# Kernel optimization log

Measured on AMD Instinct MI355X. Metric: run time of the kernel, lower is better.

The kernel has to match this reference:

```python
import jax, jax.numpy as jnp
import numpy as np

N_NODES = 100_000
N_EDGES = 3_200_000
N_FEAT = 128
N_HID = 8
N_CLASSES = 10


def setup_inputs() -> dict:
    key = jax.random.key(0)
    ks = jax.random.split(key, 16)
    g = lambda k, shape, fan_in: jax.random.normal(k, shape, jnp.float32) / np.sqrt(fan_in)
    inp = {}
    inp['x'] = jax.random.normal(ks[0], (N_NODES, N_FEAT), jnp.float32)
    inp['edge_index'] = jax.random.randint(ks[1], (2, N_EDGES), 0, N_NODES, jnp.int32)
    # lin: Linear(F, 8)
    inp['lin_w'] = g(ks[2], (N_FEAT, N_HID), N_FEAT)
    inp['lin_b'] = jnp.zeros((N_HID,), jnp.float32)
    # conv1: GATConv(8, 8, heads=2)
    inp['w1'] = g(ks[3], (N_HID, 2 * N_HID), N_HID)
    inp['a1_src'] = g(ks[4], (2, N_HID), N_HID)
    inp['a1_dst'] = g(ks[5], (2, N_HID), N_HID)
    inp['b1'] = jnp.zeros((2 * N_HID,), jnp.float32)
    # conv2: GATConv(16, 8, heads=2)
    inp['w2'] = g(ks[6], (2 * N_HID, 2 * N_HID), 2 * N_HID)
    inp['a2_src'] = g(ks[7], (2, N_HID), N_HID)
    inp['a2_dst'] = g(ks[8], (2, N_HID), N_HID)
    inp['b2'] = jnp.zeros((2 * N_HID,), jnp.float32)
    # conv3: GATConv(16, num_classes, heads=1, concat=False)
    inp['w3'] = g(ks[9], (2 * N_HID, N_CLASSES), 2 * N_HID)
    inp['a3_src'] = g(ks[10], (1, N_CLASSES), N_CLASSES)
    inp['a3_dst'] = g(ks[11], (1, N_CLASSES), N_CLASSES)
    inp['b3'] = jnp.zeros((N_CLASSES,), jnp.float32)
    return inp


def _gat_conv(x, W, a_src, a_dst, b, src, dst, heads, out_c, concat):
    """PyG GATConv with pre-appended self-loops in (src, dst)."""
    N = x.shape[0]
    xl = (x @ W).reshape(N, heads, out_c)                 # [N,H,C]
    alpha_src = (xl * a_src[None]).sum(-1)                # [N,H]
    alpha_dst = (xl * a_dst[None]).sum(-1)                # [N,H]
    e = jax.nn.leaky_relu(alpha_src[src] + alpha_dst[dst], 0.2)  # [E,H]
    # segment softmax over destination nodes
    m = jax.ops.segment_max(e, dst, num_segments=N)
    e = jnp.exp(e - m[dst])
    s = jax.ops.segment_sum(e, dst, num_segments=N)
    alpha = e / s[dst]                                    # [E,H]
    msg = xl[src] * alpha[:, :, None]                     # [E,H,C]
    out = jax.ops.segment_sum(msg, dst, num_segments=N)   # [N,H,C]
    out = out.reshape(N, heads * out_c) if concat else out.mean(axis=1)
    return out + b


def reference(x, edge_index, lin_w, lin_b, w1, a1_src, a1_dst, b1,
              w2, a2_src, a2_dst, b2, w3, a3_src, a3_dst, b3):
    N = x.shape[0]
    loops = jnp.arange(N, dtype=edge_index.dtype)
    src = jnp.concatenate([edge_index[0], loops])
    dst = jnp.concatenate([edge_index[1], loops])
    lrelu = lambda v: jax.nn.leaky_relu(v, 0.01)
    h = lrelu(x @ lin_w + lin_b)
    h = lrelu(_gat_conv(h, w1, a1_src, a1_dst, b1, src, dst, 2, N_HID, True))
    h = lrelu(_gat_conv(h, w2, a2_src, a2_dst, b2, src, dst, 2, N_HID, True))
    h = _gat_conv(h, w3, a3_src, a3_dst, b3, src, dst, 1, N_CLASSES, False)
    return jax.nn.log_softmax(h, axis=-1)
```

## Files before the change

### kernel.cpp

```cpp
#include <hip/hip_runtime.h>
#include <hip/hip_fp16.h>
#include <math.h>

#define N_NODES 100000
#define N_EDGES 3200000
#define ET (N_EDGES + N_NODES)
#define SLOT 80
#define KMAX 5
#define SHIFT 8
#define BNODES 256
#define NBUCK 391
#define BCAP 9088
#define P1_T 1024
#define E_PER 16
#define P1_WG ((N_EDGES + P1_T * E_PER - 1) / (P1_T * E_PER))
#define SCAN_T 1024
#define SCAN_CHUNK 98
#define LOG2E 1.44269504088896f

typedef _Float16 h2 __attribute__((ext_vector_type(2)));

__device__ __forceinline__ float lrelu(float v, float s) { return v > 0.f ? v : v * s; }
__device__ __forceinline__ float fexp2(float x) { return __builtin_amdgcn_exp2f(x); }

__device__ __forceinline__ h2 f2h2(float f) {
    union { float f; h2 h; } u; u.f = f; return u.h;
}

__device__ __forceinline__ float fdot2(h2 a, h2 b, float c) {
#if __has_builtin(__builtin_amdgcn_fdot2)
    return __builtin_amdgcn_fdot2(a, b, c, false);
#else
    return c + (float)a.x * (float)b.x + (float)a.y * (float)b.y;
#endif
}

template <int CTRL>
__device__ __forceinline__ float dppmov(float v) {
    return __int_as_float(__builtin_amdgcn_update_dpp(0, __float_as_int(v), CTRL, 0xF, 0xF, true));
}

__device__ __forceinline__ void reduce8(float a[8], float& ssum, int lane) {
    int b0 = lane & 1, b1 = (lane >> 1) & 1, b2 = (lane >> 2) & 1;
    float q0 = (b0 ? a[4] : a[0]) + dppmov<0xB1>(b0 ? a[0] : a[4]);
    float q1 = (b0 ? a[5] : a[1]) + dppmov<0xB1>(b0 ? a[1] : a[5]);
    float q2 = (b0 ? a[6] : a[2]) + dppmov<0xB1>(b0 ? a[2] : a[6]);
    float q3 = (b0 ? a[7] : a[3]) + dppmov<0xB1>(b0 ? a[3] : a[7]);
    float r0 = (b1 ? q2 : q0) + dppmov<0x4E>(b1 ? q0 : q2);
    float r1 = (b1 ? q3 : q1) + dppmov<0x4E>(b1 ? q1 : q3);
    float t  = (b2 ? r1 : r0) + __shfl_xor(b2 ? r0 : r1, 4, 64);
    t += __shfl_xor(t, 8, 64);
    a[0] = t;
    ssum += dppmov<0xB1>(ssum);
    ssum += dppmov<0x4E>(ssum);
    ssum += __shfl_xor(ssum, 4, 64);
    ssum += __shfl_xor(ssum, 8, 64);
}

__global__ void __launch_bounds__(P1_T) part_kernel(const int* __restrict__ ei,
                                                    int* __restrict__ bcur,
                                                    unsigned* __restrict__ pairs) {
    __shared__ int hist[NBUCK];
    __shared__ int gbase[NBUCK];
    int t = threadIdx.x;
    for (int i = t; i < NBUCK; i += P1_T) hist[i] = 0;
    __syncthreads();
    int base = blockIdx.x * (P1_T * E_PER);
    int s[E_PER], d[E_PER], r[E_PER];
#pragma unroll
    for (int k = 0; k < E_PER; k++) {
        int e = base + k * P1_T + t;
        if (e < N_EDGES) {
            s[k] = ei[e];
            d[k] = ei[N_EDGES + e];
            r[k] = atomicAdd(&hist[d[k] >> SHIFT], 1);
        }
    }
    __syncthreads();
    for (int i = t; i < NBUCK; i += P1_T)
        gbase[i] = (hist[i] > 0) ? atomicAdd(&bcur[i], hist[i]) : 0;
    __syncthreads();
#pragma unroll
    for (int k = 0; k < E_PER; k++) {
        int e = base + k * P1_T + t;
        if (e < N_EDGES) {
            int b = d[k] >> SHIFT;
            int pos = gbase[b] + r[k];
            if (pos < BCAP)
                pairs[(size_t)b * BCAP + pos] =
                    ((unsigned)(d[k] & (BNODES - 1)) << 17) | (unsigned)s[k];
        }
    }
}

__global__ void build_kernel(const int* __restrict__ bcur, const unsigned* __restrict__ pairs,
                             int* __restrict__ csr, int* __restrict__ deg) {
    __shared__ int offs[BNODES];
    int b = blockIdx.x;
    int t = threadIdx.x;
    int node0 = b << SHIFT;
    int n = node0 + t;
    if (n < N_NODES) {
        csr[n * SLOT] = n;
        offs[t] = 1;
    } else offs[t] = 0;
    __syncthreads();
    int cnt = min(bcur[b], BCAP);
    for (int i = t; i < cnt; i += BNODES) {
        unsigned v = pairs[(size_t)b * BCAP + i];
        int ln = v >> 17;
        int s = v & 0x1FFFF;
        int pos = atomicAdd(&offs[ln], 1);
        if (pos < SLOT) csr[(node0 + ln) * SLOT + pos] = s;
    }
    __syncthreads();
    if (n < N_NODES) deg[n] = offs[t];
}

__global__ void count_kernel(const int* __restrict__ ei, int* __restrict__ deg) {
    int e = blockIdx.x * blockDim.x + threadIdx.x;
    if (e >= ET) return;
    int d = (e < N_EDGES) ? ei[N_EDGES + e] : (e - N_EDGES);
    atomicAdd(&deg[d], 1);
}

__global__ void scan_kernel(const int* __restrict__ deg, int* __restrict__ rowptr,
                            int* __restrict__ cursor) {
    __shared__ int sums[SCAN_T];
    int t = threadIdx.x;
    int start = t * SCAN_CHUNK;
    int end = min(start + SCAN_CHUNK, N_NODES);
    int s = 0;
    for (int i = start; i < end; i++) s += deg[i];
    sums[t] = s;
    __syncthreads();
    for (int off = 1; off < SCAN_T; off <<= 1) {
        int v = sums[t];
        int add = (t >= off) ? sums[t - off] : 0;
        __syncthreads();
        sums[t] = v + add;
        __syncthreads();
    }
    int base = (t > 0) ? sums[t - 1] : 0;
    for (int i = start; i < end; i++) {
        rowptr[i] = base;
        cursor[i] = base;
        base += deg[i];
    }
    if (t == SCAN_T - 1) rowptr[N_NODES] = base;
}

__global__ void scatter_kernel(const int* __restrict__ ei, int* __restrict__ cursor,
                               int* __restrict__ csr) {
    int e = blockIdx.x * blockDim.x + threadIdx.x;
    if (e >= ET) return;
    int s, d;
    if (e < N_EDGES) { s = ei[e]; d = ei[N_EDGES + e]; } else { s = d = e - N_EDGES; }
    int pos = atomicAdd(&cursor[d], 1);
    csr[pos] = s;
}

template <int CIN, int H, int C, int XLS>
__global__ void prep_kernel(const float* __restrict__ hin, const float* __restrict__ W,
                            const float* __restrict__ a_src, const float* __restrict__ a_dst,
                            __half* __restrict__ xl, float* __restrict__ asrc,
                            float* __restrict__ adst) {
    __shared__ float Ws[CIN * H * C];
    __shared__ float As[H * C];
    __shared__ float Ad[H * C];
    for (int i = threadIdx.x; i < CIN * H * C; i += blockDim.x) Ws[i] = W[i];
    for (int i = threadIdx.x; i < H * C; i += blockDim.x) {
        As[i] = a_src[i] * LOG2E;
        Ad[i] = a_dst[i] * LOG2E;
    }
    __syncthreads();
    int n = blockIdx.x * blockDim.x + threadIdx.x;
    if (n >= N_NODES) return;
    float hreg[CIN];
#pragma unroll
    for (int i = 0; i < CIN; i += 4) {
        float4 v = *(const float4*)&hin[n * CIN + i];
        hreg[i] = v.x; hreg[i + 1] = v.y; hreg[i + 2] = v.z; hreg[i + 3] = v.w;
    }
#pragma unroll
    for (int h = 0; h < H; h++) {
        float as = 0.f, ad = 0.f;
#pragma unroll
        for (int c = 0; c < C; c++) {
            float v = 0.f;
#pragma unroll
            for (int i = 0; i < CIN; i++) v += hreg[i] * Ws[i * H * C + h * C + c];
            xl[n * XLS + h * C + c] = __float2half_rn(v);
            as += v * As[h * C + c];
            ad += v * Ad[h * C + c];
        }
        asrc[n * H + h] = as;
        adst[n * H + h] = ad;
    }
#pragma unroll
    for (int c = H * C; c < XLS; c++) xl[n * XLS + c] = __float2half_rn(0.f);
}

template <int H, int C, int XLS>
__global__ __launch_bounds__(256) void prep_lin_kernel(
        const float* __restrict__ x, const float* __restrict__ lw, const float* __restrict__ lb,
        const float* __restrict__ W, const float* __restrict__ a_src,
        const float* __restrict__ a_dst, __half* __restrict__ xl,
        float* __restrict__ asrc, float* __restrict__ adst) {
    __shared__ float LW[128 * 8];
    __shared__ float Ws[8 * H * C];
    __shared__ float As[H * C];
    __shared__ float Ad[H * C];
    __shared__ float Lb[8];
    for (int i = threadIdx.x; i < 128 * 8; i += 256) LW[i] = lw[i];
    for (int i = threadIdx.x; i < 8 * H * C; i += 256) Ws[i] = W[i];
    for (int i = threadIdx.x; i < H * C; i += 256) {
        As[i] = a_src[i] * LOG2E;
        Ad[i] = a_dst[i] * LOG2E;
    }
    if (threadIdx.x < 8) Lb[threadIdx.x] = lb[threadIdx.x];
    __syncthreads();
    int n = blockIdx.x * blockDim.x + threadIdx.x;
    if (n >= N_NODES) return;
    float hreg[8];
#pragma unroll
    for (int c = 0; c < 8; c++) hreg[c] = 0.f;
#pragma unroll 8
    for (int i = 0; i < 128; i += 4) {
        float4 v = *(const float4*)&x[n * 128 + i];
#pragma unroll
        for (int c = 0; c < 8; c++) hreg[c] += v.x * LW[(i + 0) * 8 + c];
#pragma unroll
        for (int c = 0; c < 8; c++) hreg[c] += v.y * LW[(i + 1) * 8 + c];
#pragma unroll
        for (int c = 0; c < 8; c++) hreg[c] += v.z * LW[(i + 2) * 8 + c];
#pragma unroll
        for (int c = 0; c < 8; c++) hreg[c] += v.w * LW[(i + 3) * 8 + c];
    }
#pragma unroll
    for (int c = 0; c < 8; c++) hreg[c] = lrelu(hreg[c] + Lb[c], 0.01f);
#pragma unroll
    for (int h = 0; h < H; h++) {
        float as = 0.f, ad = 0.f;
#pragma unroll
        for (int c = 0; c < C; c++) {
            float v = 0.f;
#pragma unroll
            for (int i = 0; i < 8; i++) v += hreg[i] * Ws[i * H * C + h * C + c];
            xl[n * XLS + h * C + c] = __float2half_rn(v);
            as += v * As[h * C + c];
            ad += v * Ad[h * C + c];
        }
        asrc[n * H + h] = as;
        adst[n * H + h] = ad;
    }
#pragma unroll
    for (int c = H * C; c < XLS; c++) xl[n * XLS + c] = __float2half_rn(0.f);
}

__global__ __launch_bounds__(256) void gat64_h2(const int* __restrict__ cnt_,
                                                const int* __restrict__ csr,
                                                const float* __restrict__ a_src,
                                                const float* __restrict__ adst,
                                                const __half* __restrict__ xl,
                                                const float* __restrict__ b,
                                                float* __restrict__ hout) {
    int wg = blockIdx.x * 4 + (threadIdx.x >> 6);
    int lane = threadIdx.x & 63;
    int eg = lane & 15;
    int q  = (lane >> 4) & 1;
    int nd = lane >> 5;
    int n = wg * 2 + nd;
    float4 as0 = *(const float4*)&a_src[q * 8];
    float4 as1 = *(const float4*)&a_src[q * 8 + 4];
    h2 av0 = {(_Float16)(as0.x * LOG2E), (_Float16)(as0.y * LOG2E)};
    h2 av1 = {(_Float16)(as0.z * LOG2E), (_Float16)(as0.w * LOG2E)};
    h2 av2 = {(_Float16)(as1.x * LOG2E), (_Float16)(as1.y * LOG2E)};
    h2 av3 = {(_Float16)(as1.z * LOG2E), (_Float16)(as1.w * LOG2E)};
    int cnt = min(cnt_[n], SLOT);
    float ad = adst[n * 2 + q];
    int idx[KMAX];
#pragma unroll
    for (int k = 0; k < KMAX; k++) {
        int i = eg + (k << 4);
        idx[k] = (i < cnt) ? csr[n * SLOT + i] : -1;
    }
    float ssum = 0.f;
    float a[8] = {0.f, 0.f, 0.f, 0.f, 0.f, 0.f, 0.f, 0.f};
#pragma unroll
    for (int k = 0; k < KMAX; k++) {
        int s = idx[k];
        if (s >= 0) {
            float4 raw = *(const float4*)&xl[s * 16 + q * 8];
            h2 x0 = f2h2(raw.x), x1 = f2h2(raw.y), x2 = f2h2(raw.z), x3 = f2h2(raw.w);
            float e = fdot2(x0, av0, fdot2(x1, av1, fdot2(x2, av2, fdot2(x3, av3, ad))));
            float w = fexp2(fmaxf(e, 0.2f * e));
            ssum += w;
            a[0] += w * (float)x0.x; a[1] += w * (float)x0.y;
            a[2] += w * (float)x1.x; a[3] += w * (float)x1.y;
            a[4] += w * (float)x2.x; a[5] += w * (float)x2.y;
            a[6] += w * (float)x3.x; a[7] += w * (float)x3.y;
        }
    }
    reduce8(a, ssum, lane);
    if ((lane & 8) == 0) {
        int ch = 8 * q + 4 * (lane & 1) + 2 * ((lane >> 1) & 1) + ((lane >> 2) & 1);
        hout[n * 16 + ch] = lrelu(a[0] / ssum + b[ch], 0.01f);
    }
}

__global__ __launch_bounds__(256) void gat64_ls(const int* __restrict__ cnt_,
                                                const int* __restrict__ csr,
                                                const float* __restrict__ a_src,
                                                const float* __restrict__ adst,
                                                const __half* __restrict__ xl,
                                                const float* __restrict__ b,
                                                float* __restrict__ out) {
    int wg = blockIdx.x * 4 + (threadIdx.x >> 6);
    int lane = threadIdx.x & 63;
    int eg = lane & 15;
    int q  = (lane >> 4) & 1;
    int nd = lane >> 5;
    int n = wg * 2 + nd;
    float avf[8];
#pragma unroll
    for (int j = 0; j < 8; j++) {
        int c = q * 8 + j;
        avf[j] = (c < 10) ? a_src[c] * LOG2E : 0.f;
    }
    h2 av0 = {(_Float16)avf[0], (_Float16)avf[1]};
    h2 av1 = {(_Float16)avf[2], (_Float16)avf[3]};
    h2 av2 = {(_Float16)avf[4], (_Float16)avf[5]};
    h2 av3 = {(_Float16)avf[6], (_Float16)avf[7]};
    int cnt = min(cnt_[n], SLOT);
    float adh = adst[n] * 0.5f;
    int idx[KMAX];
#pragma unroll
    for (int k = 0; k < KMAX; k++) {
        int i = eg + (k << 4);
        idx[k] = (i < cnt) ? csr[n * SLOT + i] : -1;
    }
    float ssum = 0.f;
    float a[8] = {0.f, 0.f, 0.f, 0.f, 0.f, 0.f, 0.f, 0.f};
#pragma unroll
    for (int k = 0; k < KMAX; k++) {
        int s = idx[k];
        if (s >= 0) {
            float4 raw = *(const float4*)&xl[s * 16 + q * 8];
            h2 x0 = f2h2(raw.x), x1 = f2h2(raw.y), x2 = f2h2(raw.z), x3 = f2h2(raw.w);
            float part = fdot2(x0, av0, fdot2(x1, av1, fdot2(x2, av2, fdot2(x3, av3, adh))));
            float e = part + __shfl_xor(part, 16, 64);
            float w = fexp2(fmaxf(e, 0.2f * e));
            ssum += w;
            a[0] += w * (float)x0.x; a[1] += w * (float)x0.y;
            a[2] += w * (float)x1.x; a[3] += w * (float)x1.y;
            a[4] += w * (float)x2.x; a[5] += w * (float)x2.y;
            a[6] += w * (float)x3.x; a[7] += w * (float)x3.y;
        }
    }
    reduce8(a, ssum, lane);
    int ch = 8 * q + 4 * (lane & 1) + 2 * ((lane >> 1) & 1) + ((lane >> 2) & 1);
    float u = (ch < 10) ? a[0] / ssum + b[ch] : -INFINITY;
    float m = u;
    m = fmaxf(m, dppmov<0xB1>(m));
    m = fmaxf(m, dppmov<0x4E>(m));
    m = fmaxf(m, __shfl_xor(m, 4, 64));
    m = fmaxf(m, __shfl_xor(m, 8, 64));
    m = fmaxf(m, __shfl_xor(m, 16, 64));
    float ex = (ch < 10 && (lane & 8) == 0) ? __expf(u - m) : 0.f;
    ex += dppmov<0xB1>(ex);
    ex += dppmov<0x4E>(ex);
    ex += __shfl_xor(ex, 4, 64);
    ex += __shfl_xor(ex, 8, 64);
    ex += __shfl_xor(ex, 16, 64);
    float lse = m + __logf(ex);
    if ((lane & 8) == 0 && ch < 10) out[n * 10 + ch] = u - lse;
}

__global__ void gat16_h2(const int* __restrict__ rowptr, const int* __restrict__ csr,
                         const float* __restrict__ asrc, const float* __restrict__ adst,
                         const __half* __restrict__ xl, const float* __restrict__ b,
                         float* __restrict__ hout) {
    int tid = blockIdx.x * blockDim.x + threadIdx.x;
    int wave = tid >> 6;
    int lane = threadIdx.x & 63;
    int g = lane >> 4;
    int c = lane & 15;
    int h = c >> 3;
    int n = wave * 4 + g;
    if (n >= N_NODES) return;
    int beg = rowptr[n], cnt = rowptr[n + 1] - beg;
    float adn = adst[n * 2 + h];
    float ssum = 0.f, pa = 0.f;
#pragma unroll 4
    for (int i = 0; i < cnt; i++) {
        int s = csr[beg + i];
        float e = asrc[s * 2 + h] + adn;
        float w = fexp2(fmaxf(e, 0.2f * e));
        ssum += w;
        pa += w * __half2float(xl[s * 16 + c]);
    }
    hout[n * 16 + c] = lrelu(pa / ssum + b[c], 0.01f);
}

__global__ void gat16_ls(const int* __restrict__ rowptr, const int* __restrict__ csr,
                         const float* __restrict__ asrc, const float* __restrict__ adst,
                         const __half* __restrict__ xl, const float* __restrict__ b,
                         float* __restrict__ out) {
    int tid = blockIdx.x * blockDim.x + threadIdx.x;
    int wave = tid >> 6;
    int lane = threadIdx.x & 63;
    int g = lane >> 4;
    int c = lane & 15;
    int n = wave * 4 + g;
    if (n >= N_NODES) return;
    int beg = rowptr[n], cnt = rowptr[n + 1] - beg;
    float adn = adst[n];
    float ssum = 0.f, pa = 0.f;
#pragma unroll 4
    for (int i = 0; i < cnt; i++) {
        int s = csr[beg + i];
        float e = asrc[s] + adn;
        float w = fexp2(fmaxf(e, 0.2f * e));
        ssum += w;
        pa += w * __half2float(xl[s * 16 + c]);
    }
    float v = pa / ssum + ((c < 10) ? b[c] : 0.f);
    float vm = (c < 10) ? v : -INFINITY;
#pragma unroll
    for (int off = 8; off >= 1; off >>= 1) vm = fmaxf(vm, __shfl_xor(vm, off, 16));
    float ex = (c < 10) ? __expf(v - vm) : 0.f;
    float sum = ex;
#pragma unroll
    for (int off = 8; off >= 1; off >>= 1) sum += __shfl_xor(sum, off, 16);
    float lse = vm + __logf(sum);
    if (c < 10) out[n * 10 + c] = v - lse;
}

extern "C" void kernel_launch(void* const* d_in, const int* in_sizes, int n_in,
                              void* d_out, int out_size, void* d_ws, size_t ws_size,
                              hipStream_t stream) {
    const float* x     = (const float*)d_in[0];
    const int*   ei    = (const int*)d_in[1];
    const float* lin_w = (const float*)d_in[2];
    const float* lin_b = (const float*)d_in[3];
    const float* w1    = (const float*)d_in[4];
    const float* a1s   = (const float*)d_in[5];
    const float* a1d   = (const float*)d_in[6];
    const float* b1    = (const float*)d_in[7];
    const float* w2    = (const float*)d_in[8];
    const float* a2s   = (const float*)d_in[9];
    const float* a2d   = (const float*)d_in[10];
    const float* b2    = (const float*)d_in[11];
    const float* w3    = (const float*)d_in[12];
    const float* a3s   = (const float*)d_in[13];
    const float* a3d   = (const float*)d_in[14];
    const float* b3    = (const float*)d_in[15];

    float* ws = (float*)d_ws;
    float* slotH  = ws;
    __half* slotX = (__half*)(ws + 1600000);
    float* as_    = ws + 3200000;
    float* ad_    = ws + 3400000;
    unsigned* pairs = (unsigned*)ws;
    int* csrP = (int*)(ws + 3600000);
    int* degP = (int*)(ws + 3600000 + N_NODES * SLOT);
    int* bcur = degP + N_NODES;
    size_t need_new = (size_t)(3600000 + N_NODES * SLOT + N_NODES + 512) * 4;

    int use_bucket = (ws_size >= need_new) ? 1 : 0;

    int* degC    = (int*)(ws + 3600000);
    int* rowptrC = degC + N_NODES;
    int* cursorC = rowptrC + N_NODES + 1;
    int* csrC    = cursorC + N_NODES;

    dim3 B(256);
    int nb_n  = (N_NODES + 255) / 256;
    int nb_et = (ET + 255) / 256;
    int nb_g  = (N_NODES + 15) / 16;
    int nb_w2 = N_NODES / 8;

    if (use_bucket) {
        hipMemsetAsync(bcur, 0, 512 * sizeof(int), stream);
        part_kernel<<<P1_WG, P1_T, 0, stream>>>(ei, bcur, pairs);
        build_kernel<<<NBUCK, BNODES, 0, stream>>>(bcur, pairs, csrP, degP);
    } else {
        hipMemsetAsync(degC, 0, N_NODES * sizeof(int), stream);
        count_kernel<<<nb_et, B, 0, stream>>>(ei, degC);
        scan_kernel<<<1, SCAN_T, 0, stream>>>(degC, rowptrC, cursorC);
        scatter_kernel<<<nb_et, B, 0, stream>>>(ei, cursorC, csrC);
    }

    prep_lin_kernel<2, 8, 16><<<nb_n, B, 0, stream>>>(x, lin_w, lin_b, w1, a1s, a1d,
                                                      slotX, as_, ad_);
    if (use_bucket) gat64_h2<<<nb_w2, B, 0, stream>>>(degP, csrP, a1s, ad_, slotX, b1, slotH);
    else            gat16_h2<<<nb_g, B, 0, stream>>>(rowptrC, csrC, as_, ad_, slotX, b1, slotH);

    prep_kernel<16, 2, 8, 16><<<nb_n, B, 0, stream>>>(slotH, w2, a2s, a2d, slotX, as_, ad_);
    if (use_bucket) gat64_h2<<<nb_w2, B, 0, stream>>>(degP, csrP, a2s, ad_, slotX, b2, slotH);
    else            gat16_h2<<<nb_g, B, 0, stream>>>(rowptrC, csrC, as_, ad_, slotX, b2, slotH);

    prep_kernel<16, 1, 10, 16><<<nb_n, B, 0, stream>>>(slotH, w3, a3s, a3d, slotX, as_, ad_);
    if (use_bucket) gat64_ls<<<nb_w2, B, 0, stream>>>(degP, csrP, a3s, ad_, slotX, b3, (float*)d_out);
    else            gat16_ls<<<nb_g, B, 0, stream>>>(rowptrC, csrC, as_, ad_, slotX, b3, (float*)d_out);
}
```

Baseline: 280.9 us.

## Replace two-pass bucketed CSR build with direct atomic slot scatter

The two-pass graph build (a bucket partition kernel with shared-memory histograms, then a per-bucket build kernel) is replaced by one kernel in which each edge atomically bumps its destination's degree and writes its source into a fixed-width slot row. The self-loop is no longer stored in the slot array; the GAT kernels add it implicitly as index zero and shift the stored neighbours by one. This removes a kernel launch and the intermediate pairs buffer, but relies on scattered global atomics across 100k counters and uncoalesced writes into the slot array.

```diff
diff --git a/kernel.cpp b/kernel.cpp
--- a/kernel.cpp
+++ b/kernel.cpp
@@ -7,13 +7,6 @@
 #define ET (N_EDGES + N_NODES)
 #define SLOT 80
 #define KMAX 5
-#define SHIFT 8
-#define BNODES 256
-#define NBUCK 391
-#define BCAP 9088
-#define P1_T 1024
-#define E_PER 16
-#define P1_WG ((N_EDGES + P1_T * E_PER - 1) / (P1_T * E_PER))
 #define SCAN_T 1024
 #define SCAN_CHUNK 98
 #define LOG2E 1.44269504088896f
@@ -57,64 +50,14 @@
     ssum += __shfl_xor(ssum, 8, 64);
 }
 
-__global__ void __launch_bounds__(P1_T) part_kernel(const int* __restrict__ ei,
-                                                    int* __restrict__ bcur,
-                                                    unsigned* __restrict__ pairs) {
-    __shared__ int hist[NBUCK];
-    __shared__ int gbase[NBUCK];
-    int t = threadIdx.x;
-    for (int i = t; i < NBUCK; i += P1_T) hist[i] = 0;
-    __syncthreads();
-    int base = blockIdx.x * (P1_T * E_PER);
-    int s[E_PER], d[E_PER], r[E_PER];
-#pragma unroll
-    for (int k = 0; k < E_PER; k++) {
-        int e = base + k * P1_T + t;
-        if (e < N_EDGES) {
-            s[k] = ei[e];
-            d[k] = ei[N_EDGES + e];
-            r[k] = atomicAdd(&hist[d[k] >> SHIFT], 1);
-        }
-    }
-    __syncthreads();
-    for (int i = t; i < NBUCK; i += P1_T)
-        gbase[i] = (hist[i] > 0) ? atomicAdd(&bcur[i], hist[i]) : 0;
-    __syncthreads();
-#pragma unroll
-    for (int k = 0; k < E_PER; k++) {
-        int e = base + k * P1_T + t;
-        if (e < N_EDGES) {
-            int b = d[k] >> SHIFT;
-            int pos = gbase[b] + r[k];
-            if (pos < BCAP)
-                pairs[(size_t)b * BCAP + pos] =
-                    ((unsigned)(d[k] & (BNODES - 1)) << 17) | (unsigned)s[k];
-        }
-    }
-}
-
-__global__ void build_kernel(const int* __restrict__ bcur, const unsigned* __restrict__ pairs,
-                             int* __restrict__ csr, int* __restrict__ deg) {
-    __shared__ int offs[BNODES];
-    int b = blockIdx.x;
-    int t = threadIdx.x;
-    int node0 = b << SHIFT;
-    int n = node0 + t;
-    if (n < N_NODES) {
-        csr[n * SLOT] = n;
-        offs[t] = 1;
-    } else offs[t] = 0;
-    __syncthreads();
-    int cnt = min(bcur[b], BCAP);
-    for (int i = t; i < cnt; i += BNODES) {
-        unsigned v = pairs[(size_t)b * BCAP + i];
-        int ln = v >> 17;
-        int s = v & 0x1FFFF;
-        int pos = atomicAdd(&offs[ln], 1);
-        if (pos < SLOT) csr[(node0 + ln) * SLOT + pos] = s;
-    }
-    __syncthreads();
-    if (n < N_NODES) deg[n] = offs[t];
+__global__ void scatter_slot(const int* __restrict__ ei, int* __restrict__ deg,
+                             int* __restrict__ csr) {
+    int e = blockIdx.x * blockDim.x + threadIdx.x;
+    if (e >= N_EDGES) return;
+    int s = ei[e];
+    int d = ei[N_EDGES + e];
+    int pos = atomicAdd(&deg[d], 1);
+    if (pos < SLOT - 1) csr[d * SLOT + pos] = s;
 }
 
 __global__ void count_kernel(const int* __restrict__ ei, int* __restrict__ deg) {
@@ -277,13 +220,14 @@
     h2 av1 = {(_Float16)(as0.z * LOG2E), (_Float16)(as0.w * LOG2E)};
     h2 av2 = {(_Float16)(as1.x * LOG2E), (_Float16)(as1.y * LOG2E)};
     h2 av3 = {(_Float16)(as1.z * LOG2E), (_Float16)(as1.w * LOG2E)};
-    int cnt = min(cnt_[n], SLOT);
+    int cnt = min(cnt_[n] + 1, SLOT);
     float ad = adst[n * 2 + q];
     int idx[KMAX];
 #pragma unroll
     for (int k = 0; k < KMAX; k++) {
         int i = eg + (k << 4);
-        idx[k] = (i < cnt) ? csr[n * SLOT + i] : -1;
+        int j = i ? i - 1 : 0;
+        idx[k] = (i < cnt) ? (i ? csr[n * SLOT + j] : n) : -1;
     }
     float ssum = 0.f;
     float a[8] = {0.f, 0.f, 0.f, 0.f, 0.f, 0.f, 0.f, 0.f};
@@ -332,13 +276,14 @@
     h2 av1 = {(_Float16)avf[2], (_Float16)avf[3]};
     h2 av2 = {(_Float16)avf[4], (_Float16)avf[5]};
     h2 av3 = {(_Float16)avf[6], (_Float16)avf[7]};
-    int cnt = min(cnt_[n], SLOT);
+    int cnt = min(cnt_[n] + 1, SLOT);
     float adh = adst[n] * 0.5f;
     int idx[KMAX];
 #pragma unroll
     for (int k = 0; k < KMAX; k++) {
         int i = eg + (k << 4);
-        idx[k] = (i < cnt) ? csr[n * SLOT + i] : -1;
+        int j = i ? i - 1 : 0;
+        idx[k] = (i < cnt) ? (i ? csr[n * SLOT + j] : n) : -1;
     }
     float ssum = 0.f;
     float a[8] = {0.f, 0.f, 0.f, 0.f, 0.f, 0.f, 0.f, 0.f};
@@ -462,10 +407,8 @@
     __half* slotX = (__half*)(ws + 1600000);
     float* as_    = ws + 3200000;
     float* ad_    = ws + 3400000;
-    unsigned* pairs = (unsigned*)ws;
     int* csrP = (int*)(ws + 3600000);
     int* degP = (int*)(ws + 3600000 + N_NODES * SLOT);
-    int* bcur = degP + N_NODES;
     size_t need_new = (size_t)(3600000 + N_NODES * SLOT + N_NODES + 512) * 4;
 
     int use_bucket = (ws_size >= need_new) ? 1 : 0;
@@ -477,14 +420,14 @@
 
     dim3 B(256);
     int nb_n  = (N_NODES + 255) / 256;
+    int nb_e  = (N_EDGES + 255) / 256;
     int nb_et = (ET + 255) / 256;
     int nb_g  = (N_NODES + 15) / 16;
     int nb_w2 = N_NODES / 8;
 
     if (use_bucket) {
-        hipMemsetAsync(bcur, 0, 512 * sizeof(int), stream);
-        part_kernel<<<P1_WG, P1_T, 0, stream>>>(ei, bcur, pairs);
-        build_kernel<<<NBUCK, BNODES, 0, stream>>>(bcur, pairs, csrP, degP);
+        hipMemsetAsync(degP, 0, N_NODES * sizeof(int), stream);
+        scatter_slot<<<nb_e, B, 0, stream>>>(ei, degP, csrP);
     } else {
         hipMemsetAsync(degC, 0, N_NODES * sizeof(int), stream);
         count_kernel<<<nb_et, B, 0, stream>>>(ei, degC);
```

Measured after the change: 498.6 us. 77.5% more time.
